# Kernel tuning notes

Hardware: AMD Instinct MI355X
Metric: run time of the kernel (lower is better)

The kernel has to match this reference:

```python
import jax, jax.numpy as jnp
import numpy as np

DIM = 2048
HEAD_DIM = 128
H = DIM // HEAD_DIM          # num ttt heads = 16
D_H = 128                    # inter_multi = 1.0 -> d_h = head_dim
CHUNK = 2048                 # lact_chunk_size
B, L = 1, 8192
BASE_LR = 0.01
LN_EPS = 1e-6                # flax LayerNorm default
NS_COEFS = [(4.0848, -6.8946, 2.927), (3.9505, -6.3029, 2.6377),
            (3.7418, -5.5913, 2.3037), (2.8769, -3.1427, 1.2046),
            (2.8366, -3.0525, 1.2012)]


def silu(x):
    return x * jax.nn.sigmoid(x)


def silu_backprop(dy, x):
    s = jax.nn.sigmoid(x)
    return dy * s * (1 + x * (1 - s))


def l2_norm(x, eps=1e-5):
    return x / (jnp.linalg.norm(x, axis=-1, keepdims=True) + eps)


def zeropower_ns5(G):
    # 5-step Newton-Schulz orthogonalization on a batch of matrices (bh, m, n)
    X = G
    transposed = G.shape[1] > G.shape[2]
    if transposed:
        X = jnp.swapaxes(X, 1, 2)
    X = X / (jnp.linalg.norm(X, axis=(1, 2), keepdims=True) + 1e-7)
    for a, b, c in NS_COEFS:
        A = X @ jnp.swapaxes(X, 1, 2)
        Bm = b * A + c * (A @ A)
        X = a * X + Bm @ X
    if transposed:
        X = jnp.swapaxes(X, 1, 2)
    return X


def block_causal_lact_swiglu(w0, w1, w2, q, k, v, lr0, lr1, lr2, momentum):
    # w0,w2: (bh, d_h, d); w1: (bh, d, d_h); q,k,v: (bh, l, d); lr*: (bh, l, 1)
    bh, l, d = k.shape
    v = jnp.swapaxes(v, 1, 2)   # (bh, d, l)
    q = jnp.swapaxes(q, 1, 2)   # (bh, d, l)
    w0_norm = jnp.linalg.norm(w0, axis=2, keepdims=True)
    w1_norm = jnp.linalg.norm(w1, axis=2, keepdims=True)
    w2_norm = jnp.linalg.norm(w2, axis=2, keepdims=True)
    outs = []
    for i in range(0, l - CHUNK, CHUNK):
        s, e = i, i + CHUNK
        ki = k[:, s:e, :]                      # (bh, C, d)
        vi = v[:, :, s:e]                      # (bh, d, C)
        qi = q[:, :, s:e]                      # (bh, d, C)
        lr0i, lr1i, lr2i = lr0[:, s:e, :], lr1[:, s:e, :], lr2[:, s:e, :]
        # apply current fast weights to queries
        h = w2 @ qi                            # (bh, d_h, C)
        gate = silu(w0 @ qi)
        outs.append(w1 @ (gate * h))           # (bh, d, C)
        # manual SwiGLU backprop through keys to get fast-weight grads
        kiT = jnp.swapaxes(ki, 1, 2)           # (bh, d, C)
        gate_before = w0 @ kiT                 # (bh, d_h, C)
        hidden_before = w2 @ kiT               # (bh, d_h, C)
        hidden = silu(gate_before) * hidden_before
        dhidden = jnp.swapaxes(w1, 1, 2) @ vi  # (bh, d_h, C)
        dhidden_before = dhidden * silu(gate_before)
        dgate = dhidden * hidden_before
        dgate_before = silu_backprop(dgate, gate_before)
        lr1iT = jnp.swapaxes(lr1i, 1, 2)       # (bh, 1, C) per-token lr
        dw1 = vi @ jnp.swapaxes(hidden * lr1iT, 1, 2)   # (bh, d, d_h)
        dw0 = dgate_before @ (ki * lr0i)                # (bh, d_h, d)
        dw2 = dhidden_before @ (ki * lr2i)              # (bh, d_h, d)
        if momentum is not None:
            m_i = jnp.mean(momentum[:, s:e, :], axis=1, keepdims=True)  # (bh,1,1)
            dw0 = dw0 + dw0 * m_i
            dw1 = dw1 + dw1 * m_i
            dw2 = dw2 + dw2 * m_i
        dw0 = zeropower_ns5(dw0)
        dw1 = zeropower_ns5(dw1)
        dw2 = zeropower_ns5(dw2)
        w0 = w0 + dw0
        w1 = w1 + dw1
        w2 = w2 + dw2
        # renormalize rows back to the initial norms
        w0 = w0 / (jnp.linalg.norm(w0, axis=2, keepdims=True) + 1e-5) * w0_norm
        w1 = w1 / (jnp.linalg.norm(w1, axis=2, keepdims=True) + 1e-5) * w1_norm
        w2 = w2 / (jnp.linalg.norm(w2, axis=2, keepdims=True) + 1e-5) * w2_norm
    # final chunk: apply only
    qi = q[:, :, l - CHUNK:]
    h = w2 @ qi
    gate = silu(w0 @ qi)
    outs.append(w1 @ (gate * h))
    out = jnp.concatenate(outs, axis=2)        # (bh, d, l)
    return jnp.swapaxes(out, 1, 2)             # (bh, l, d)


def _forward(x, W_qkv, W_lr, W_o, W_m, b_m, W_s, b_s, ln_g, ln_b, w0, w1, w2):
    b, l, _ = x.shape
    h, d = H, HEAD_DIM
    qkv = silu(x @ W_qkv).reshape(b, l, h, 3 * d)
    ttt_q, ttt_k, ttt_v = jnp.split(qkv, 3, axis=-1)
    ttt_q = l2_norm(ttt_q).reshape(b * h, l, d)
    ttt_k = l2_norm(ttt_k).reshape(b * h, l, d)
    ttt_v = ttt_v.reshape(b * h, l, d)
    base_lr_inv = BASE_LR + jnp.log(-jnp.expm1(jnp.float32(-BASE_LR)))
    lr = jax.nn.softplus(x @ W_lr + base_lr_inv)                 # (b, l, 3h)
    lr = lr.reshape(b, l, 3, h).transpose(2, 0, 3, 1).reshape(3, b * h, l, 1)
    lr0, lr1, lr2 = lr[0], lr[1], lr[2]
    w0b = jnp.tile(w0, (b, 1, 1))
    w1b = jnp.tile(w1, (b, 1, 1))
    w2b = jnp.tile(w2, (b, 1, 1))
    momentum = jax.nn.sigmoid(x @ W_m + b_m)                     # (b, l, h)
    momentum = momentum.reshape(b, l, h, 1).transpose(0, 2, 1, 3).reshape(b * h, l, 1)
    out = block_causal_lact_swiglu(w0b, w1b, w2b, ttt_q, ttt_k, ttt_v,
                                   lr0, lr1, lr2, momentum)      # (bh, l, d)
    # LayerNorm over last dim (flax default eps)
    mu = jnp.mean(out, axis=-1, keepdims=True)
    var = jnp.mean(jnp.square(out - mu), axis=-1, keepdims=True)
    out = (out - mu) * jax.lax.rsqrt(var + LN_EPS) * ln_g + ln_b
    scale = silu(x @ W_s + b_s).reshape(b, l, h, 1).transpose(0, 2, 1, 3).reshape(b * h, l, 1)
    out = out * scale
    out = out.reshape(b, h, l, d).transpose(0, 2, 1, 3).reshape(b, l, h * d)
    return out @ W_o


def setup_inputs() -> dict:
    ks = jax.random.split(jax.random.key(0), 11)
    sd = 1.0 / np.sqrt(DIM)
    return {
        "x": jax.random.normal(ks[0], (B, L, DIM), jnp.float32),
        "W_qkv": jax.random.normal(ks[1], (DIM, 3 * DIM), jnp.float32) * sd,
        "W_lr": jax.random.normal(ks[2], (DIM, 3 * H), jnp.float32) * sd,
        "W_o": jax.random.normal(ks[3], (DIM, DIM), jnp.float32) * sd,
        "W_m": jax.random.normal(ks[4], (DIM, H), jnp.float32) * sd,
        "b_m": jnp.zeros((H,), jnp.float32),
        "W_s": jax.random.normal(ks[5], (DIM, H), jnp.float32) * sd,
        "b_s": jnp.zeros((H,), jnp.float32),
        "ln_g": jnp.ones((HEAD_DIM,), jnp.float32),
        "ln_b": jnp.zeros((HEAD_DIM,), jnp.float32),
        "w0": jax.random.normal(ks[6], (H, D_H, HEAD_DIM), jnp.float32) / np.sqrt(HEAD_DIM),
        "w1": jax.random.normal(ks[7], (H, HEAD_DIM, D_H), jnp.float32) / np.sqrt(D_H),
        "w2": jax.random.normal(ks[8], (H, D_H, HEAD_DIM), jnp.float32) / np.sqrt(HEAD_DIM),
    }


def reference(x, W_qkv, W_lr, W_o, W_m, b_m, W_s, b_s, ln_g, ln_b, w0, w1, w2):
    return _forward(x, W_qkv, W_lr, W_o, W_m, b_m, W_s, b_s, ln_g, ln_b, w0, w1, w2)
```

## Files before the change

### kernel.cpp

```cpp
#include <hip/hip_runtime.h>
#include <hip/hip_bf16.h>
#include <cstdint>
#include <cstddef>

#define LSEQ   8192
#define DMODEL 2048
#define NH     16
#define HD     128
#define CH     2048

typedef __attribute__((ext_vector_type(8))) __bf16 bf16x8;
typedef __attribute__((ext_vector_type(4))) float f32x4;


__device__ __forceinline__ float wave_sum64(float v) {
#pragma unroll
  for (int m = 32; m; m >>= 1) v += __shfl_xor(v, m, 64);
  return v;
}

__device__ __forceinline__ float sigm(float x) { return 1.0f / (1.0f + expf(-x)); }

__device__ __forceinline__ unsigned short f2bf(float f) {
  unsigned int u = __float_as_uint(f);
  u += 0x7FFFu + ((u >> 16) & 1u);
  return (unsigned short)(u >> 16);
}
__device__ __forceinline__ float bf2f(unsigned short h) {
  return __uint_as_float((unsigned int)h << 16);
}

__device__ __forceinline__ void gload_lds16(const void* g, void* l) {
  __builtin_amdgcn_global_load_lds((__attribute__((address_space(1))) void*)(g),
                                   (__attribute__((address_space(3))) void*)(l), 16, 0, 0);
}


__global__ void k_cast(const float* __restrict__ X, unsigned short* __restrict__ Xb, int n4) {
  int i = blockIdx.x * 256 + threadIdx.x;
  int stride = gridDim.x * 256;
  for (; i < n4; i += stride) {
    float4 v = ((const float4*)X)[i];
    ushort4 o;
    o.x = f2bf(v.x); o.y = f2bf(v.y); o.z = f2bf(v.z); o.w = f2bf(v.w);
    ((ushort4*)Xb)[i] = o;
  }
}

__global__ void k_tcast(const float* __restrict__ W, unsigned short* __restrict__ Wt,
                        int K, int N) {
  __shared__ float t[64][65];
  const int n0 = blockIdx.x * 64, k0 = blockIdx.y * 64;
  const int tid = threadIdx.x;
  const int cx = tid & 63, ry = tid >> 6;
#pragma unroll
  for (int r = 0; r < 16; ++r) {
    int row = ry + r * 4;
    t[row][cx] = W[(size_t)(k0 + row) * N + n0 + cx];
  }
  __syncthreads();
#pragma unroll
  for (int r = 0; r < 16; ++r) {
    int nn = ry + r * 4;
    Wt[(size_t)(n0 + nn) * K + k0 + cx] = f2bf(t[cx][nn]);
  }
}


__device__ __forceinline__ void gemm_core(const unsigned short* __restrict__ A,
                                          const unsigned short* __restrict__ B,
                                          int K, int ldA, int ldB, int row0, int col0,
                                          unsigned short* Al, unsigned short* Bl,
                                          f32x4 acc[4][4]) {
  const int tid = threadIdx.x;
  const int w = tid >> 6, l = tid & 63;
  const int lrow = l & 15, lk = (l >> 4) * 8;
  const int wr = (w >> 1) * 64, wc = (w & 1) * 64;
  const int srow = l >> 2, skk = (l & 3) * 8;

  for (int kk = 0; kk < K; kk += 32) {
#pragma unroll
    for (int q = 0; q < 2; ++q) {
      int c = w * 2 + q;
      gload_lds16(A + (size_t)(row0 + c * 16 + srow) * ldA + kk + skk, &Al[c * 512]);
      gload_lds16(B + (size_t)(col0 + c * 16 + srow) * ldB + kk + skk, &Bl[c * 512]);
    }
    __syncthreads();
    bf16x8 af[4], bfr[4];
#pragma unroll
    for (int m = 0; m < 4; ++m)
      af[m] = *(const bf16x8*)&Al[(wr + m * 16 + lrow) * 32 + lk];
#pragma unroll
    for (int n = 0; n < 4; ++n)
      bfr[n] = *(const bf16x8*)&Bl[(wc + n * 16 + lrow) * 32 + lk];
#pragma unroll
    for (int m = 0; m < 4; ++m)
#pragma unroll
      for (int n = 0; n < 4; ++n)
        acc[m][n] = __builtin_amdgcn_mfma_f32_16x16x32_bf16(af[m], bfr[n], acc[m][n], 0, 0, 0);
    __syncthreads();
  }
}


__device__ __forceinline__ bf16x8 ld_sw(const unsigned short* base, int row, int kcol) {
  int byte = (row * 256 + kcol * 2) ^ ((row & 7) << 4);
  return *(const bf16x8*)((const char*)base + byte);
}
__device__ __forceinline__ void st_sw(unsigned short* base, int row, int col, unsigned short v) {
  int byte = (row * 256 + col * 2) ^ ((row & 7) << 4);
  *(unsigned short*)((char*)base + byte) = v;
}

__device__ __forceinline__ void stage_sw(const float* __restrict__ src, int ld,
                                         unsigned short* dst, int tid) {
#pragma unroll
  for (int p = 0; p < 16; ++p) {
    int row = p * 8 + (tid >> 5);
    int col = (tid & 31) * 4;
    float4 v = *(const float4*)(src + (size_t)row * ld + col);
    int byte = (row * 256 + col * 2) ^ ((row & 7) << 4);
    unsigned short* d = (unsigned short*)((char*)dst + byte);
    d[0] = f2bf(v.x); d[1] = f2bf(v.y); d[2] = f2bf(v.z); d[3] = f2bf(v.w);
  }
}

__device__ __forceinline__ void stage_hl(const float* __restrict__ src, int ld,
                                         unsigned short* H, unsigned short* L, int tid) {
#pragma unroll
  for (int p = 0; p < 16; ++p) {
    int row = p * 8 + (tid >> 5);
    int col = (tid & 31) * 4;
    float4 v = *(const float4*)(src + (size_t)row * ld + col);
    int byte = (row * 256 + col * 2) ^ ((row & 7) << 4);
    unsigned short* h = (unsigned short*)((char*)H + byte);
    unsigned short* l = (unsigned short*)((char*)L + byte);
    const float* pv = (const float*)&v;
#pragma unroll
    for (int i = 0; i < 4; ++i) {
      unsigned short hi = f2bf(pv[i]);
      h[i] = hi;
      l[i] = f2bf(pv[i] - bf2f(hi));
    }
  }
}

__device__ __forceinline__ void stage_hl_t(const float* __restrict__ src, int ld,
                                           unsigned short* H, unsigned short* L, int tid) {
#pragma unroll
  for (int p = 0; p < 16; ++p) {
    int k = p * 8 + (tid >> 5);
    int c = (tid & 31) * 4;
    float4 v = *(const float4*)(src + (size_t)k * ld + c);
    const float* pv = (const float*)&v;
#pragma unroll
    for (int i = 0; i < 4; ++i) {
      unsigned short hi = f2bf(pv[i]);
      st_sw(H, c + i, k, hi);
      st_sw(L, c + i, k, f2bf(pv[i] - bf2f(hi)));
    }
  }
}

__device__ __forceinline__ void stage_hl_ts(const float* __restrict__ src, int ld,
                                            const float* __restrict__ lr,
                                            unsigned short* H, unsigned short* L, int tid) {
#pragma unroll
  for (int p = 0; p < 16; ++p) {
    int t = p * 8 + (tid >> 5);
    int d = (tid & 31) * 4;
    float4 v = *(const float4*)(src + (size_t)t * ld + d);
    float sc = lr[t];
    const float* pv = (const float*)&v;
#pragma unroll
    for (int i = 0; i < 4; ++i) {
      float x = pv[i] * sc;
      unsigned short hi = f2bf(x);
      st_sw(H, d + i, t, hi);
      st_sw(L, d + i, t, f2bf(x - bf2f(hi)));
    }
  }
}


__global__ void k_init_w(const float* __restrict__ w0, const float* __restrict__ w1,
                         const float* __restrict__ w2, float* __restrict__ WW,
                         float* __restrict__ WN0) {
  int rid = blockIdx.x;
  int m = rid >> 11;
  int gr = rid & 2047;
  const float* src = (m == 0) ? w0 : (m == 1) ? w1 : w2;
  const float* row = src + (size_t)gr * HD;
  float* drow = WW + ((size_t)m * 2048 + gr) * HD;
  int l = threadIdx.x;
  float v0 = row[l], v1 = row[l + 64];
  drow[l] = v0; drow[l + 64] = v1;
  float s = wave_sum64(v0 * v0 + v1 * v1);
  if (l == 0) WN0[rid] = sqrtf(s);
}


__global__ __launch_bounds__(256) void k_qkv_mfma(const unsigned short* __restrict__ xb,
                                                  const unsigned short* __restrict__ Wqt,
                                                  float* __restrict__ Q, float* __restrict__ Km,
                                                  float* __restrict__ V) {
  __shared__ unsigned short Al[128 * 32];
  __shared__ unsigned short Bl[128 * 32];
  f32x4 acc[4][4];
#pragma unroll
  for (int m = 0; m < 4; ++m)
#pragma unroll
    for (int n = 0; n < 4; ++n) acc[m][n] = {};

  gemm_core(xb, Wqt, DMODEL, DMODEL, DMODEL, blockIdx.x * 128, blockIdx.y * 128, Al, Bl, acc);

  const int ct = blockIdx.y, hh = ct / 3, which = ct % 3;
  float* dst = (which == 0) ? Q : (which == 1) ? Km : V;
  const int tid = threadIdx.x, w = tid >> 6, l = tid & 63;
  const int wr = (w >> 1) * 64, wc = (w & 1) * 64;
#pragma unroll
  for (int m = 0; m < 4; ++m)
#pragma unroll
    for (int j = 0; j < 4; ++j) {
      int t = blockIdx.x * 128 + wr + m * 16 + (l >> 4) * 4 + j;
      int fth = t * NH + hh;
      int g = fth >> 13, tp = fth & 8191;
      float* drow = dst + ((size_t)g * LSEQ + tp) * HD;
#pragma unroll
      for (int n = 0; n < 4; ++n) {
        float v = acc[m][n][j];
        drow[wc + n * 16 + (l & 15)] = v * sigm(v);
      }
    }
}

__global__ void k_l2norm(float* __restrict__ Q, float* __restrict__ Km) {
  int rid = blockIdx.x * 4 + (threadIdx.x >> 6);
  int l = threadIdx.x & 63;
  float* base = (rid < NH * LSEQ) ? Q : Km;
  int r = (rid < NH * LSEQ) ? rid : rid - NH * LSEQ;
  float* row = base + (size_t)r * HD;
  float v0 = row[l], v1 = row[l + 64];
  float s = wave_sum64(v0 * v0 + v1 * v1);
  float f = 1.0f / (sqrtf(s) + 1e-5f);
  row[l] = v0 * f;
  row[l + 64] = v1 * f;
}


// ... 150 lines not shown
    for (int m = 0; m < 4; ++m)
#pragma unroll
      for (int n = 0; n < 4; ++n)
        oa[m][n] = __builtin_amdgcn_mfma_f32_16x16x32_bf16(af[m], b1[n], oa[m][n], 0, 0, 0);
  }
  __syncthreads();
#pragma unroll
  for (int m = 0; m < 4; ++m)
#pragma unroll
    for (int n = 0; n < 4; ++n)
#pragma unroll
      for (int j = 0; j < 4; ++j) {
        int row = wr + m * 16 + (l >> 4) * 4 + j;
        int col = wc + n * 16 + (l & 15);
        Os[row * 132 + col] = oa[m][n][j];
      }
  __syncthreads();

  const int tok = tid >> 1, part = tid & 1;
  const float* orow = Os + tok * 132 + part * 64;
  float sum = 0.0f;
#pragma unroll
  for (int q = 0; q < 16; ++q) {
    float4 v = *(const float4*)(orow + q * 4);
    sum += (v.x + v.y) + (v.z + v.w);
  }
  sum += __shfl_xor(sum, 1, 64);
  float mu = sum * (1.0f / 128.0f);
  float vs = 0.0f;
#pragma unroll
  for (int q = 0; q < 16; ++q) {
    float4 v = *(const float4*)(orow + q * 4);
    float d0 = v.x - mu, d1 = v.y - mu, d2 = v.z - mu, d3 = v.w - mu;
    vs += d0 * d0 + d1 * d1 + d2 * d2 + d3 * d3;
  }
  vs += __shfl_xor(vs, 1, 64);
  float rstd = rsqrtf(vs * (1.0f / 128.0f) + 1e-6f);
  int tabs = s + t0 + tok;
  float sc = SCL[(size_t)g * LSEQ + tabs];
  unsigned short* urow = U + (size_t)tabs * DMODEL + g * HD + part * 64;
#pragma unroll
  for (int q = 0; q < 16; ++q) {
    float4 v = *(const float4*)(orow + q * 4);
    int d = part * 64 + q * 4;
    ushort4 o;
    o.x = f2bf(((v.x - mu) * rstd * lng[d + 0] + lnb[d + 0]) * sc);
    o.y = f2bf(((v.y - mu) * rstd * lng[d + 1] + lnb[d + 1]) * sc);
    o.z = f2bf(((v.z - mu) * rstd * lng[d + 2] + lnb[d + 2]) * sc);
    o.w = f2bf(((v.w - mu) * rstd * lng[d + 3] + lnb[d + 3]) * sc);
    *(ushort4*)(urow + q * 4) = o;
  }
}


__global__ __launch_bounds__(256) void k_front_mx(const float* __restrict__ WW,
                                                  const float* __restrict__ Km,
                                                  const float* __restrict__ V,
                                                  float* __restrict__ BUF, int s) {
  __shared__ __align__(16) char smem[131072];
  unsigned short* AH = (unsigned short*)smem;
  unsigned short* AL = (unsigned short*)(smem + 32768);
  unsigned short* BH = (unsigned short*)(smem + 65536);
  unsigned short* BL = (unsigned short*)(smem + 98304);

  const int tt0 = blockIdx.x * 128;
  const int g = blockIdx.y;
  const int z = blockIdx.z;
  const int tid = threadIdx.x;
  const int w = tid >> 6, l = tid & 63;
  const int lrow = l & 15, lk8 = (l >> 4) * 8;
  const int wr = (w >> 1) * 64, wc = (w & 1) * 64;

  const int wsel = (z == 0) ? 0 : (z == 1) ? 2 : 1;
  const float* wg = WW + ((size_t)wsel * 2048 + g * 128) * 128;
  const float* X = (z == 2) ? V : Km;

  if (z != 2) stage_hl(wg, 128, AH, AL, tid);
  else        stage_hl_t(wg, 128, AH, AL, tid);
  stage_hl(X + ((size_t)g * LSEQ + s + tt0) * HD, HD, BH, BL, tid);
  __syncthreads();

  f32x4 acc[4][4];
#pragma unroll
  for (int m = 0; m < 4; ++m)
#pragma unroll
    for (int n = 0; n < 4; ++n) acc[m][n] = {};
#pragma unroll
  for (int kk = 0; kk < 128; kk += 32) {
    bf16x8 ah[4], al4[4], bh[4], bl4[4];
#pragma unroll
    for (int m = 0; m < 4; ++m) {
      ah[m] = ld_sw(AH, wr + m * 16 + lrow, kk + lk8);
      al4[m] = ld_sw(AL, wr + m * 16 + lrow, kk + lk8);
    }
#pragma unroll
    for (int n = 0; n < 4; ++n) {
      bh[n] = ld_sw(BH, wc + n * 16 + lrow, kk + lk8);
      bl4[n] = ld_sw(BL, wc + n * 16 + lrow, kk + lk8);
    }
#pragma unroll
    for (int m = 0; m < 4; ++m)
#pragma unroll
      for (int n = 0; n < 4; ++n) {
        acc[m][n] = __builtin_amdgcn_mfma_f32_16x16x32_bf16(ah[m], bh[n], acc[m][n], 0, 0, 0);
        acc[m][n] = __builtin_amdgcn_mfma_f32_16x16x32_bf16(ah[m], bl4[n], acc[m][n], 0, 0, 0);
        acc[m][n] = __builtin_amdgcn_mfma_f32_16x16x32_bf16(al4[m], bh[n], acc[m][n], 0, 0, 0);
      }
  }

  float* out = BUF + (size_t)z * (NH * 128 * CH) + (size_t)g * 128 * CH;
#pragma unroll
  for (int m = 0; m < 4; ++m)
#pragma unroll
    for (int n = 0; n < 4; ++n)
#pragma unroll
      for (int j = 0; j < 4; ++j) {
        int row = wr + m * 16 + (l >> 4) * 4 + j;
        int col = wc + n * 16 + (l & 15);
        out[(size_t)row * CH + tt0 + col] = acc[m][n][j];
      }
}

__global__ void k_elem(float* __restrict__ BA, float* __restrict__ BB, float* __restrict__ BC) {
  size_t i = ((size_t)blockIdx.x * 256 + threadIdx.x) * 4;
  float4 a = *(const float4*)(BA + i);
  float4 b = *(const float4*)(BB + i);
  float4 c = *(const float4*)(BC + i);
  float4 ha, hb2, hc;
  float* pa = (float*)&a; float* pb = (float*)&b; float* pc = (float*)&c;
  float* oa = (float*)&ha; float* ob = (float*)&hb2; float* oc = (float*)&hc;
#pragma unroll
  for (int k = 0; k < 4; ++k) {
    float gb = pa[k], hb = pb[k], dh = pc[k];
    float sg = sigm(gb);
    float sgb = gb * sg;
    float hid = sgb * hb;
    float dgate = dh * hb;
    float dgb = dgate * sg * (1.0f + gb * (1.0f - sg));
    float dhb = dh * sgb;
    oa[k] = hid; ob[k] = dgb; oc[k] = dhb;
  }
  *(float4*)(BA + i) = ha;
  *(float4*)(BB + i) = hb2;
  *(float4*)(BC + i) = hc;
}

__global__ __launch_bounds__(256) void k_dwp_mx(const float* __restrict__ BUF,
                                                const float* __restrict__ Km,
                                                const float* __restrict__ V,
                                                const float* __restrict__ LR,
                                                float* __restrict__ DWP, int s) {
  __shared__ __align__(16) char smem[131072];
  unsigned short* AH = (unsigned short*)smem;
  unsigned short* AL = (unsigned short*)(smem + 32768);
  unsigned short* BH = (unsigned short*)(smem + 65536);
  unsigned short* BL = (unsigned short*)(smem + 98304);

  const int p = blockIdx.x;
  const int g = blockIdx.y;
  const int z = blockIdx.z;
  const int tid = threadIdx.x;
  const int w = tid >> 6, l = tid & 63;
  const int lrow = l & 15, lk8 = (l >> 4) * 8;
  const int wr = (w >> 1) * 64, wc = (w & 1) * 64;

  const int msel = (z == 0) ? 1 : (z == 1) ? 0 : 2;
  const float* M = BUF + (size_t)msel * (NH * 128 * CH) + (size_t)g * 128 * CH;
  const float* N = (z == 1) ? V : Km;
  const float* lr = LR + (size_t)(z * NH + g) * LSEQ;
  const int ts = p * 256;

  f32x4 acc[4][4];
#pragma unroll
  for (int m = 0; m < 4; ++m)
#pragma unroll
    for (int n = 0; n < 4; ++n) acc[m][n] = {};

  for (int h = 0; h < 2; ++h) {
    if (h) __syncthreads();
    stage_hl(M + ts + h * 128, CH, AH, AL, tid);
    stage_hl_ts(N + ((size_t)g * LSEQ + s + ts + h * 128) * HD, HD,
                lr + s + ts + h * 128, BH, BL, tid);
    __syncthreads();
#pragma unroll
    for (int kk = 0; kk < 128; kk += 32) {
      bf16x8 ah[4], al4[4], bh[4], bl4[4];
#pragma unroll
      for (int m = 0; m < 4; ++m) {
        ah[m] = ld_sw(AH, wr + m * 16 + lrow, kk + lk8);
        al4[m] = ld_sw(AL, wr + m * 16 + lrow, kk + lk8);
      }
#pragma unroll
      for (int n = 0; n < 4; ++n) {
        bh[n] = ld_sw(BH, wc + n * 16 + lrow, kk + lk8);
        bl4[n] = ld_sw(BL, wc + n * 16 + lrow, kk + lk8);
      }
#pragma unroll
      for (int m = 0; m < 4; ++m)
#pragma unroll
        for (int n = 0; n < 4; ++n) {
          acc[m][n] = __builtin_amdgcn_mfma_f32_16x16x32_bf16(ah[m], bh[n], acc[m][n], 0, 0, 0);
          acc[m][n] = __builtin_amdgcn_mfma_f32_16x16x32_bf16(ah[m], bl4[n], acc[m][n], 0, 0, 0);
          acc[m][n] = __builtin_amdgcn_mfma_f32_16x16x32_bf16(al4[m], bh[n], acc[m][n], 0, 0, 0);
        }
    }
  }

  float* outp = DWP + (((size_t)(z * NH + g)) * 8 + p) * 16384;
#pragma unroll
  for (int m = 0; m < 4; ++m)
#pragma unroll
    for (int n = 0; n < 4; ++n)
#pragma unroll
      for (int j = 0; j < 4; ++j) {
        int row = wr + m * 16 + (l >> 4) * 4 + j;
        int col = wc + n * 16 + (l & 15);
        outp[row * 128 + col] = acc[m][n][j];
      }
}

__global__ void k_dwred(const float* __restrict__ DWP, float* __restrict__ DW) {
  int zg = blockIdx.x;
  int z = zg >> 4;
  const float* base = DWP + (size_t)zg * 8 * 16384;
  float* out = DW + (size_t)zg * 16384;
  for (int idx = threadIdx.x; idx < 16384; idx += 256) {
    float sv = 0.0f;
#pragma unroll
    for (int pp = 0; pp < 8; ++pp) sv += base[(size_t)pp * 16384 + idx];
    int oidx = (z == 1) ? ((idx & 127) * 128 + (idx >> 7)) : idx;
    out[oidx] = sv;
  }
}


__global__ __launch_bounds__(1024) void k_ns5(float* __restrict__ DW) {
  __shared__ float Xs[128 * 128];
  __shared__ float Aw[128 * 128];
  const float NA[5] = {4.0848f, 3.9505f, 3.7418f, 2.8769f, 2.8366f};
  const float NB[5] = {-6.8946f, -6.3029f, -5.5913f, -3.1427f, -3.0525f};
  const float NC[5] = {2.927f, 2.6377f, 2.3037f, 1.2046f, 1.2012f};
  float* Gm = DW + (size_t)blockIdx.x * 16384;
  const int tid = threadIdx.x;
  const int ty = tid >> 5, tx = tid & 31;

  float psum = 0.0f;
#pragma unroll
  for (int r = 0; r < 16; ++r) {
    int idx = tid + r * 1024;
    float v = Gm[idx];
    Xs[idx] = v;
    psum = fmaf(v, v, psum);
  }
  psum = wave_sum64(psum);
  if ((tid & 63) == 0) Aw[tid >> 6] = psum;
  __syncthreads();
  if (tid == 0) {
    float tot = 0.0f;
    for (int i = 0; i < 16; ++i) tot += Aw[i];
    Aw[0] = 1.0f / (sqrtf(tot) + 1e-7f);
  }
  __syncthreads();
  float scl = Aw[0];
#pragma unroll
  for (int r = 0; r < 16; ++r) {
    int idx = tid + r * 1024;
    Xs[idx] *= scl;
  }
  __syncthreads();

#pragma unroll 1
  for (int it = 0; it < 5; ++it) {
    float ac = NA[it], bc = NB[it], cc = NC[it];
#pragma unroll
    for (int ii = 0; ii < 4; ++ii)
#pragma unroll
      for (int jj = 0; jj < 4; ++jj)
        Aw[(tx * 4 + jj) * 128 + ty * 4 + ii] = Xs[(ty * 4 + ii) * 128 + tx * 4 + jj];
    __syncthreads();
    float Ar[4][4];
#pragma unroll
    for (int ii = 0; ii < 4; ++ii)
#pragma unroll
      for (int jj = 0; jj < 4; ++jj) Ar[ii][jj] = 0.0f;
    for (int k = 0; k < 128; ++k) {
      float a[4], b[4];
#pragma unroll
      for (int ii = 0; ii < 4; ++ii) a[ii] = Xs[(ty * 4 + ii) * 128 + k];
#pragma unroll
      for (int jj = 0; jj < 4; ++jj) b[jj] = Aw[k * 128 + tx * 4 + jj];
#pragma unroll
      for (int ii = 0; ii < 4; ++ii)
#pragma unroll
        for (int jj = 0; jj < 4; ++jj) Ar[ii][jj] = fmaf(a[ii], b[jj], Ar[ii][jj]);
    }
    __syncthreads();
#pragma unroll
    for (int ii = 0; ii < 4; ++ii)
#pragma unroll
      for (int jj = 0; jj < 4; ++jj)
        Aw[(ty * 4 + ii) * 128 + tx * 4 + jj] = Ar[ii][jj];
    __syncthreads();
    float Bm[4][4];
#pragma unroll
    for (int ii = 0; ii < 4; ++ii)
#pragma unroll
      for (int jj = 0; jj < 4; ++jj) Bm[ii][jj] = 0.0f;
    for (int k = 0; k < 128; ++k) {
      float a[4], b[4];
#pragma unroll
      for (int ii = 0; ii < 4; ++ii) a[ii] = Aw[(ty * 4 + ii) * 128 + k];
#pragma unroll
      for (int jj = 0; jj < 4; ++jj) b[jj] = Aw[k * 128 + tx * 4 + jj];
#pragma unroll
      for (int ii = 0; ii < 4; ++ii)
#pragma unroll
        for (int jj = 0; jj < 4; ++jj) Bm[ii][jj] = fmaf(a[ii], b[jj], Bm[ii][jj]);
    }
#pragma unroll
    for (int ii = 0; ii < 4; ++ii)
#pragma unroll
      for (int jj = 0; jj < 4; ++jj) Bm[ii][jj] = fmaf(bc, Ar[ii][jj], cc * Bm[ii][jj]);
    __syncthreads();
#pragma unroll
    for (int ii = 0; ii < 4; ++ii)
#pragma unroll
      for (int jj = 0; jj < 4; ++jj)
        Aw[(ty * 4 + ii) * 128 + tx * 4 + jj] = Bm[ii][jj];
    __syncthreads();
    float Xn[4][4];
#pragma unroll
    for (int ii = 0; ii < 4; ++ii)
#pragma unroll
      for (int jj = 0; jj < 4; ++jj)
        Xn[ii][jj] = ac * Xs[(ty * 4 + ii) * 128 + tx * 4 + jj];
    for (int k = 0; k < 128; ++k) {
      float a[4], b[4];
#pragma unroll
      for (int ii = 0; ii < 4; ++ii) a[ii] = Aw[(ty * 4 + ii) * 128 + k];
#pragma unroll
      for (int jj = 0; jj < 4; ++jj) b[jj] = Xs[k * 128 + tx * 4 + jj];
#pragma unroll
      for (int ii = 0; ii < 4; ++ii)
#pragma unroll
        for (int jj = 0; jj < 4; ++jj) Xn[ii][jj] = fmaf(a[ii], b[jj], Xn[ii][jj]);
    }
    __syncthreads();
#pragma unroll
    for (int ii = 0; ii < 4; ++ii)
#pragma unroll
      for (int jj = 0; jj < 4; ++jj)
        Xs[(ty * 4 + ii) * 128 + tx * 4 + jj] = Xn[ii][jj];
    __syncthreads();
  }
#pragma unroll
  for (int r = 0; r < 16; ++r) {
    int idx = tid + r * 1024;
    Gm[idx] = Xs[idx];
  }
}

__global__ void k_apply(float* __restrict__ WW, const float* __restrict__ DW,
                        const float* __restrict__ WN0) {
  int rid = blockIdx.x;
  int l = threadIdx.x;
  float* wrow = WW + (size_t)rid * 128;
  const float* drow = DW + (size_t)rid * 128;
  float v0 = wrow[l] + drow[l];
  float v1 = wrow[l + 64] + drow[l + 64];
  float s = wave_sum64(v0 * v0 + v1 * v1);
  float f = WN0[rid] / (sqrtf(s) + 1e-5f);
  wrow[l] = v0 * f;
  wrow[l + 64] = v1 * f;
}


__global__ __launch_bounds__(256) void k_final_mfma(const unsigned short* __restrict__ U,
                                                    const unsigned short* __restrict__ Wot,
                                                    float* __restrict__ out) {
  __shared__ unsigned short Al[128 * 32];
  __shared__ unsigned short Bl[128 * 32];
  f32x4 acc[4][4];
#pragma unroll
  for (int m = 0; m < 4; ++m)
#pragma unroll
    for (int n = 0; n < 4; ++n) acc[m][n] = {};

  const int row0 = blockIdx.x * 128, col0 = blockIdx.y * 128;
  gemm_core(U, Wot, DMODEL, DMODEL, DMODEL, row0, col0, Al, Bl, acc);

  const int tid = threadIdx.x, w = tid >> 6, l = tid & 63;
  const int wr = (w >> 1) * 64, wc = (w & 1) * 64;
#pragma unroll
  for (int m = 0; m < 4; ++m)
#pragma unroll
    for (int j = 0; j < 4; ++j) {
      int t = row0 + wr + m * 16 + (l >> 4) * 4 + j;
      float* orow = out + (size_t)t * DMODEL + col0;
#pragma unroll
      for (int n = 0; n < 4; ++n)
        orow[wc + n * 16 + (l & 15)] = acc[m][n][j];
    }
}


extern "C" void kernel_launch(void* const* d_in, const int* in_sizes, int n_in,
                              void* d_out, int out_size, void* d_ws, size_t ws_size,
                              hipStream_t stream) {
  (void)in_sizes; (void)n_in; (void)out_size;
  const float* x    = (const float*)d_in[0];
  const float* Wqkv = (const float*)d_in[1];
  const float* Wlr  = (const float*)d_in[2];
  const float* Wo   = (const float*)d_in[3];
  const float* Wsc  = (const float*)d_in[6];
  const float* bs   = (const float*)d_in[7];
  const float* lng  = (const float*)d_in[8];
  const float* lnb  = (const float*)d_in[9];
  const float* w0   = (const float*)d_in[10];
  const float* w1   = (const float*)d_in[11];
  const float* w2   = (const float*)d_in[12];

  float* Q = (float*)d_out;

  float* ws = (float*)d_ws;
  size_t off = 0;
  auto alloc = [&](size_t n) { float* p = ws + off; off += n; return p; };
  float* Km   = alloc((size_t)NH * LSEQ * HD);
  float* V    = alloc((size_t)NH * LSEQ * HD);
  float* Uf   = alloc((size_t)LSEQ * DMODEL / 2);
  float* LR   = alloc((size_t)3 * NH * LSEQ);
  float* SCL  = alloc((size_t)NH * LSEQ);
  float* WW   = alloc((size_t)3 * NH * HD * HD);
  float* WN0  = alloc((size_t)3 * NH * HD);
  float* BUF  = alloc((size_t)3 * NH * HD * CH);
  float* DW   = alloc((size_t)3 * NH * HD * HD);
  float* DWP  = alloc((size_t)3 * NH * 8 * HD * HD);
  if (off * sizeof(float) > ws_size) return;

  unsigned short* U = (unsigned short*)Uf;
  unsigned short* xb  = (unsigned short*)BUF;
  unsigned short* Wqt = (unsigned short*)(BUF + (size_t)LSEQ * DMODEL / 2);
  float* Plr = BUF;
  unsigned short* Wot = (unsigned short*)BUF;

  k_init_w<<<3 * NH * HD, 64, 0, stream>>>(w0, w1, w2, WW, WN0);
  k_cast<<<2048, 256, 0, stream>>>(x, xb, LSEQ * DMODEL / 4);
  k_tcast<<<dim3(3 * DMODEL / 64, DMODEL / 64), 256, 0, stream>>>(Wqkv, Wqt, DMODEL, 3 * DMODEL);
  k_qkv_mfma<<<dim3(LSEQ / 128, 48), 256, 0, stream>>>(xb, Wqt, Q, Km, V);
  k_l2norm<<<2 * NH * LSEQ / 4, 256, 0, stream>>>(Q, Km);
  k_lrms5<<<dim3(LSEQ / 64, 16), 256, 0, stream>>>(x, Wlr, Wsc, Plr);
  k_lrsum<<<LSEQ * 64 / 256, 256, 0, stream>>>(Plr, bs, LR, SCL);

  for (int c = 0; c < 4; ++c) {
    int s = c * CH;
    k_out2<<<dim3(CH / 128, NH), 256, 0, stream>>>(WW, Q, SCL, lng, lnb, U, s);
    if (c < 3) {
      k_front_mx<<<dim3(CH / 128, NH, 3), 256, 0, stream>>>(WW, Km, V, BUF, s);
      k_elem<<<(NH * HD * CH) / (256 * 4), 256, 0, stream>>>(
          BUF, BUF + (size_t)NH * HD * CH, BUF + (size_t)2 * NH * HD * CH);
      k_dwp_mx<<<dim3(8, NH, 3), 256, 0, stream>>>(BUF, Km, V, LR, DWP, s);
      k_dwred<<<3 * NH, 256, 0, stream>>>(DWP, DW);
      k_ns5<<<3 * NH, 1024, 0, stream>>>(DW);
      k_apply<<<3 * NH * HD, 64, 0, stream>>>(WW, DW, WN0);
    }
  }
  k_tcast<<<dim3(DMODEL / 64, DMODEL / 64), 256, 0, stream>>>(Wo, Wot, DMODEL, DMODEL);
  k_final_mfma<<<dim3(LSEQ / 128, DMODEL / 128), 256, 0, stream>>>(U, Wot, (float*)d_out);
}
```

Baseline: 1.594 ms.

## Fuse front GEMMs with SwiGLU elementwise and move NS5 onto MFMA

Merges the three front-pass GEMMs (w0·k, w2·k, w1ᵀ·v) into one 1024-thread kernel. That kernel computes the SwiGLU forward and backward elementwise terms in registers, which removes the separate k_elem pass and its global round trip over BUF. A transposed copy of w1 is kept up to date in init and apply so the w1 operand can be read row-major. The Newton-Schulz orthogonalization is rewritten from scalar FP32 LDS matmuls to bf16 hi/lo split MFMA, which trades some precision for matrix-core throughput. The NS5 kernel also adds an in-LDS transpose each iteration.

```diff
diff --git a/kernel.cpp b/kernel.cpp
--- a/kernel.cpp
+++ b/kernel.cpp
@@ -34,6 +34,8 @@
   __builtin_amdgcn_global_load_lds((__attribute__((address_space(1))) void*)(g),
                                    (__attribute__((address_space(3))) void*)(l), 16, 0, 0);
 }
+
+union bfu8 { bf16x8 v; unsigned short u[8]; };
 
 
 __global__ void k_cast(const float* __restrict__ X, unsigned short* __restrict__ Xb, int n4) {
@@ -111,6 +113,10 @@
   int byte = (row * 256 + col * 2) ^ ((row & 7) << 4);
   *(unsigned short*)((char*)base + byte) = v;
 }
+__device__ __forceinline__ unsigned short ld_sw1(const unsigned short* base, int row, int col) {
+  int byte = (row * 256 + col * 2) ^ ((row & 7) << 4);
+  return *(const unsigned short*)((const char*)base + byte);
+}
 
 __device__ __forceinline__ void stage_sw(const float* __restrict__ src, int ld,
                                          unsigned short* dst, int tid) {
@@ -145,19 +151,22 @@
   }
 }
 
-__device__ __forceinline__ void stage_hl_t(const float* __restrict__ src, int ld,
-                                           unsigned short* H, unsigned short* L, int tid) {
-#pragma unroll
-  for (int p = 0; p < 16; ++p) {
-    int k = p * 8 + (tid >> 5);
-    int c = (tid & 31) * 4;
-    float4 v = *(const float4*)(src + (size_t)k * ld + c);
+__device__ __forceinline__ void stage_hl_1024(const float* __restrict__ src, int ld,
+                                              unsigned short* H, unsigned short* L, int tid) {
+#pragma unroll
+  for (int p = 0; p < 4; ++p) {
+    int row = p * 32 + (tid >> 5);
+    int col = (tid & 31) * 4;
+    float4 v = *(const float4*)(src + (size_t)row * ld + col);
+    int byte = (row * 256 + col * 2) ^ ((row & 7) << 4);
+    unsigned short* h = (unsigned short*)((char*)H + byte);
+    unsigned short* l = (unsigned short*)((char*)L + byte);
     const float* pv = (const float*)&v;
 #pragma unroll
     for (int i = 0; i < 4; ++i) {
       unsigned short hi = f2bf(pv[i]);
-      st_sw(H, c + i, k, hi);
-      st_sw(L, c + i, k, f2bf(pv[i] - bf2f(hi)));
+      h[i] = hi;
+      l[i] = f2bf(pv[i] - bf2f(hi));
     }
   }
 }
@@ -185,7 +194,7 @@
 
 __global__ void k_init_w(const float* __restrict__ w0, const float* __restrict__ w1,
                          const float* __restrict__ w2, float* __restrict__ WW,
-                         float* __restrict__ WN0) {
+                         float* __restrict__ WN0, float* __restrict__ W1T) {
   int rid = blockIdx.x;
   int m = rid >> 11;
   int gr = rid & 2047;
@@ -195,6 +204,11 @@
   int l = threadIdx.x;
   float v0 = row[l], v1 = row[l + 64];
   drow[l] = v0; drow[l + 64] = v1;
+  if (m == 1) {
+    int g = gr >> 7, r = gr & 127;
+    W1T[((size_t)g * 128 + l) * 128 + r] = v0;
+    W1T[((size_t)g * 128 + l + 64) * 128 + r] = v1;
+  }
   float s = wave_sum64(v0 * v0 + v1 * v1);
   if (l == 0) WN0[rid] = sqrtf(s);
 }
@@ -451,97 +465,107 @@
   }
 }
 
-
-__global__ __launch_bounds__(256) void k_front_mx(const float* __restrict__ WW,
-                                                  const float* __restrict__ Km,
-                                                  const float* __restrict__ V,
-                                                  float* __restrict__ BUF, int s) {
+__global__ __launch_bounds__(1024) void k_fe(const float* __restrict__ WW,
+                                             const float* __restrict__ W1T,
+                                             const float* __restrict__ Km,
+                                             const float* __restrict__ V,
+                                             float* __restrict__ BUF, int s) {
   __shared__ __align__(16) char smem[131072];
-  unsigned short* AH = (unsigned short*)smem;
-  unsigned short* AL = (unsigned short*)(smem + 32768);
-  unsigned short* BH = (unsigned short*)(smem + 65536);
-  unsigned short* BL = (unsigned short*)(smem + 98304);
+  unsigned short* KH = (unsigned short*)smem;
+  unsigned short* KL = (unsigned short*)(smem + 32768);
+  unsigned short* VH = (unsigned short*)(smem + 65536);
+  unsigned short* VL = (unsigned short*)(smem + 98304);
 
   const int tt0 = blockIdx.x * 128;
   const int g = blockIdx.y;
-  const int z = blockIdx.z;
   const int tid = threadIdx.x;
   const int w = tid >> 6, l = tid & 63;
+  const int ww = w >> 2, wv = w & 3;
   const int lrow = l & 15, lk8 = (l >> 4) * 8;
-  const int wr = (w >> 1) * 64, wc = (w & 1) * 64;
-
-  const int wsel = (z == 0) ? 0 : (z == 1) ? 2 : 1;
-  const float* wg = WW + ((size_t)wsel * 2048 + g * 128) * 128;
-  const float* X = (z == 2) ? V : Km;
-
-  if (z != 2) stage_hl(wg, 128, AH, AL, tid);
-  else        stage_hl_t(wg, 128, AH, AL, tid);
-  stage_hl(X + ((size_t)g * LSEQ + s + tt0) * HD, HD, BH, BL, tid);
-  __syncthreads();
-
-  f32x4 acc[4][4];
-#pragma unroll
-  for (int m = 0; m < 4; ++m)
-#pragma unroll
-    for (int n = 0; n < 4; ++n) acc[m][n] = {};
-#pragma unroll
-  for (int kk = 0; kk < 128; kk += 32) {
-    bf16x8 ah[4], al4[4], bh[4], bl4[4];
-#pragma unroll
-    for (int m = 0; m < 4; ++m) {
-      ah[m] = ld_sw(AH, wr + m * 16 + lrow, kk + lk8);
-      al4[m] = ld_sw(AL, wr + m * 16 + lrow, kk + lk8);
-    }
-#pragma unroll
-    for (int n = 0; n < 4; ++n) {
-      bh[n] = ld_sw(BH, wc + n * 16 + lrow, kk + lk8);
-      bl4[n] = ld_sw(BL, wc + n * 16 + lrow, kk + lk8);
-    }
-#pragma unroll
-    for (int m = 0; m < 4; ++m)
-#pragma unroll
-      for (int n = 0; n < 4; ++n) {
-        acc[m][n] = __builtin_amdgcn_mfma_f32_16x16x32_bf16(ah[m], bh[n], acc[m][n], 0, 0, 0);
-        acc[m][n] = __builtin_amdgcn_mfma_f32_16x16x32_bf16(ah[m], bl4[n], acc[m][n], 0, 0, 0);
-        acc[m][n] = __builtin_amdgcn_mfma_f32_16x16x32_bf16(al4[m], bh[n], acc[m][n], 0, 0, 0);
-      }
-  }
-
-  float* out = BUF + (size_t)z * (NH * 128 * CH) + (size_t)g * 128 * CH;
-#pragma unroll
-  for (int m = 0; m < 4; ++m)
-#pragma unroll
-    for (int n = 0; n < 4; ++n)
+  const int frow = (l >> 4) * 4, fcol = l & 15;
+
+  stage_hl_1024(Km + ((size_t)g * LSEQ + s + tt0) * HD, HD, KH, KL, tid);
+  stage_hl_1024(V + ((size_t)g * LSEQ + s + tt0) * HD, HD, VH, VL, tid);
+  __syncthreads();
+
+  const float* Asrc[3];
+  Asrc[0] = WW + ((size_t)0 * 2048 + g * 128) * 128;
+  Asrc[1] = WW + ((size_t)2 * 2048 + g * 128) * 128;
+  Asrc[2] = W1T + (size_t)g * 16384;
+
+  f32x4 acc[3][2][2];
+#pragma unroll
+  for (int q = 0; q < 3; ++q)
+#pragma unroll
+    for (int m = 0; m < 2; ++m)
+#pragma unroll
+      for (int n = 0; n < 2; ++n) acc[q][m][n] = {};
+
+#pragma unroll 1
+  for (int q = 0; q < 3; ++q) {
+    const float* src = Asrc[q];
+    const unsigned short* BH = (q == 2) ? VH : KH;
+    const unsigned short* BL = (q == 2) ? VL : KL;
+#pragma unroll
+    for (int kk = 0; kk < 128; kk += 32) {
+      bf16x8 ah[2], al[2], bh[2], bl[2];
+#pragma unroll
+      for (int m = 0; m < 2; ++m) {
+        int row = ww * 32 + m * 16 + lrow;
+        float4 v0 = *(const float4*)(src + (size_t)row * 128 + kk + lk8);
+        float4 v1 = *(const float4*)(src + (size_t)row * 128 + kk + lk8 + 4);
+        bfu8 h, lo;
+        const float* p0 = (const float*)&v0;
+        const float* p1 = (const float*)&v1;
+#pragma unroll
+        for (int i = 0; i < 4; ++i) {
+          unsigned short hb0 = f2bf(p0[i]);
+          h.u[i] = hb0; lo.u[i] = f2bf(p0[i] - bf2f(hb0));
+          unsigned short hb1 = f2bf(p1[i]);
+          h.u[i + 4] = hb1; lo.u[i + 4] = f2bf(p1[i] - bf2f(hb1));
+        }
+        ah[m] = h.v; al[m] = lo.v;
+      }
+#pragma unroll
+      for (int n = 0; n < 2; ++n) {
+        int row = wv * 32 + n * 16 + lrow;
+        bh[n] = ld_sw(BH, row, kk + lk8);
+        bl[n] = ld_sw(BL, row, kk + lk8);
+      }
+#pragma unroll
+      for (int m = 0; m < 2; ++m)
+#pragma unroll
+        for (int n = 0; n < 2; ++n) {
+          acc[q][m][n] = __builtin_amdgcn_mfma_f32_16x16x32_bf16(ah[m], bh[n], acc[q][m][n], 0, 0, 0);
+          acc[q][m][n] = __builtin_amdgcn_mfma_f32_16x16x32_bf16(ah[m], bl[n], acc[q][m][n], 0, 0, 0);
+          acc[q][m][n] = __builtin_amdgcn_mfma_f32_16x16x32_bf16(al[m], bh[n], acc[q][m][n], 0, 0, 0);
+        }
+    }
+  }
+
+  float* out0 = BUF + (size_t)0 * (NH * 128 * CH) + (size_t)g * 128 * CH;
+  float* out1 = BUF + (size_t)1 * (NH * 128 * CH) + (size_t)g * 128 * CH;
+  float* out2 = BUF + (size_t)2 * (NH * 128 * CH) + (size_t)g * 128 * CH;
+#pragma unroll
+  for (int m = 0; m < 2; ++m)
+#pragma unroll
+    for (int n = 0; n < 2; ++n)
 #pragma unroll
       for (int j = 0; j < 4; ++j) {
-        int row = wr + m * 16 + (l >> 4) * 4 + j;
-        int col = wc + n * 16 + (l & 15);
-        out[(size_t)row * CH + tt0 + col] = acc[m][n][j];
-      }
-}
-
-__global__ void k_elem(float* __restrict__ BA, float* __restrict__ BB, float* __restrict__ BC) {
-  size_t i = ((size_t)blockIdx.x * 256 + threadIdx.x) * 4;
-  float4 a = *(const float4*)(BA + i);
-  float4 b = *(const float4*)(BB + i);
-  float4 c = *(const float4*)(BC + i);
-  float4 ha, hb2, hc;
-  float* pa = (float*)&a; float* pb = (float*)&b; float* pc = (float*)&c;
-  float* oa = (float*)&ha; float* ob = (float*)&hb2; float* oc = (float*)&hc;
-#pragma unroll
-  for (int k = 0; k < 4; ++k) {
-    float gb = pa[k], hb = pb[k], dh = pc[k];
-    float sg = sigm(gb);
-    float sgb = gb * sg;
-    float hid = sgb * hb;
-    float dgate = dh * hb;
-    float dgb = dgate * sg * (1.0f + gb * (1.0f - sg));
-    float dhb = dh * sgb;
-    oa[k] = hid; ob[k] = dgb; oc[k] = dhb;
-  }
-  *(float4*)(BA + i) = ha;
-  *(float4*)(BB + i) = hb2;
-  *(float4*)(BC + i) = hc;
+        int row = ww * 32 + m * 16 + frow + j;
+        int col = wv * 32 + n * 16 + fcol;
+        float gb = acc[0][m][n][j];
+        float hb = acc[1][m][n][j];
+        float dh = acc[2][m][n][j];
+        float sg = sigm(gb);
+        float sgb = gb * sg;
+        float hid = sgb * hb;
+        float dgate = dh * hb;
+        float dgb = dgate * sg * (1.0f + gb * (1.0f - sg));
+        float dhb = dh * sgb;
+        size_t o = (size_t)row * CH + tt0 + col;
+        out0[o] = hid; out1[o] = dgb; out2[o] = dhb;
+      }
 }
 
 __global__ __launch_bounds__(256) void k_dwp_mx(const float* __restrict__ BUF,
@@ -632,136 +656,230 @@
   }
 }
 
-
-__global__ __launch_bounds__(1024) void k_ns5(float* __restrict__ DW) {
-  __shared__ float Xs[128 * 128];
-  __shared__ float Aw[128 * 128];
+__global__ __launch_bounds__(1024) void k_ns5_mfma(float* __restrict__ DW) {
+  __shared__ __align__(16) char smem[131072];
+  unsigned short* PH = (unsigned short*)smem;
+  unsigned short* PL = (unsigned short*)(smem + 32768);
+  unsigned short* QH = (unsigned short*)(smem + 65536);
+  unsigned short* QL = (unsigned short*)(smem + 98304);
+  float* red = (float*)(smem + 65536);
+
   const float NA[5] = {4.0848f, 3.9505f, 3.7418f, 2.8769f, 2.8366f};
   const float NB[5] = {-6.8946f, -6.3029f, -5.5913f, -3.1427f, -3.0525f};
   const float NC[5] = {2.927f, 2.6377f, 2.3037f, 1.2046f, 1.2012f};
   float* Gm = DW + (size_t)blockIdx.x * 16384;
   const int tid = threadIdx.x;
-  const int ty = tid >> 5, tx = tid & 31;
-
+  const int w = tid >> 6, l = tid & 63;
+  const int ww = w >> 2, wv = w & 3;
+  const int lrow = l & 15, lk8 = (l >> 4) * 8;
+  const int frow = (l >> 4) * 4, fcol = l & 15;
+
+  float vals[16];
   float psum = 0.0f;
+#pragma unroll
+  for (int r = 0; r < 16; ++r) {
+    vals[r] = Gm[tid + r * 1024];
+    psum = fmaf(vals[r], vals[r], psum);
+  }
+  psum = wave_sum64(psum);
+  if (l == 0) red[w] = psum;
+  __syncthreads();
+  float tot = 0.0f;
+#pragma unroll
+  for (int i = 0; i < 16; ++i) tot += red[i];
+  float scl = 1.0f / (sqrtf(tot) + 1e-7f);
+  __syncthreads();
 #pragma unroll
   for (int r = 0; r < 16; ++r) {
     int idx = tid + r * 1024;
-    float v = Gm[idx];
-    Xs[idx] = v;
-    psum = fmaf(v, v, psum);
-  }
-  psum = wave_sum64(psum);
-  if ((tid & 63) == 0) Aw[tid >> 6] = psum;
-  __syncthreads();
-  if (tid == 0) {
-    float tot = 0.0f;
-    for (int i = 0; i < 16; ++i) tot += Aw[i];
-    Aw[0] = 1.0f / (sqrtf(tot) + 1e-7f);
-  }
-  __syncthreads();
-  float scl = Aw[0];
+    int rr = idx >> 7, cc = idx & 127;
+    float v = vals[r] * scl;
+    unsigned short hi = f2bf(v);
+    st_sw(PH, rr, cc, hi);
+    st_sw(PL, rr, cc, f2bf(v - bf2f(hi)));
+  }
+  __syncthreads();
+
+#pragma unroll 1
+  for (int it = 0; it < 5; ++it) {
+    const float ac = NA[it], bc = NB[it], cc2 = NC[it];
+
+    f32x4 accA[2][2];
+#pragma unroll
+    for (int m = 0; m < 2; ++m)
+#pragma unroll
+      for (int n = 0; n < 2; ++n) accA[m][n] = {};
+#pragma unroll
+    for (int kk = 0; kk < 128; kk += 32) {
+      bf16x8 ah[2], al[2], bh[2], bl[2];
+#pragma unroll
+      for (int m = 0; m < 2; ++m) {
+        ah[m] = ld_sw(PH, ww * 32 + m * 16 + lrow, kk + lk8);
+        al[m] = ld_sw(PL, ww * 32 + m * 16 + lrow, kk + lk8);
+      }
+#pragma unroll
+      for (int n = 0; n < 2; ++n) {
+        bh[n] = ld_sw(PH, wv * 32 + n * 16 + lrow, kk + lk8);
+        bl[n] = ld_sw(PL, wv * 32 + n * 16 + lrow, kk + lk8);
+      }
+#pragma unroll
+      for (int m = 0; m < 2; ++m)
+#pragma unroll
+        for (int n = 0; n < 2; ++n) {
+          accA[m][n] = __builtin_amdgcn_mfma_f32_16x16x32_bf16(ah[m], bh[n], accA[m][n], 0, 0, 0);
+          accA[m][n] = __builtin_amdgcn_mfma_f32_16x16x32_bf16(ah[m], bl[n], accA[m][n], 0, 0, 0);
+          accA[m][n] = __builtin_amdgcn_mfma_f32_16x16x32_bf16(al[m], bh[n], accA[m][n], 0, 0, 0);
+        }
+    }
+#pragma unroll
+    for (int m = 0; m < 2; ++m)
+#pragma unroll
+      for (int n = 0; n < 2; ++n)
+#pragma unroll
+        for (int j = 0; j < 4; ++j) {
+          int row = ww * 32 + m * 16 + frow + j;
+          int col = wv * 32 + n * 16 + fcol;
+          float v = accA[m][n][j];
+          unsigned short hi = f2bf(v);
+          st_sw(QH, row, col, hi);
+          st_sw(QL, row, col, f2bf(v - bf2f(hi)));
+        }
+    __syncthreads();
+
+    f32x4 accB[2][2];
+#pragma unroll
+    for (int m = 0; m < 2; ++m)
+#pragma unroll
+      for (int n = 0; n < 2; ++n) accB[m][n] = {};
+#pragma unroll
+    for (int kk = 0; kk < 128; kk += 32) {
+      bf16x8 ah[2], al[2], bh[2], bl[2];
+#pragma unroll
+      for (int m = 0; m < 2; ++m) {
+        ah[m] = ld_sw(QH, ww * 32 + m * 16 + lrow, kk + lk8);
+        al[m] = ld_sw(QL, ww * 32 + m * 16 + lrow, kk + lk8);
+      }
+#pragma unroll
+      for (int n = 0; n < 2; ++n) {
+        bh[n] = ld_sw(QH, wv * 32 + n * 16 + lrow, kk + lk8);
+        bl[n] = ld_sw(QL, wv * 32 + n * 16 + lrow, kk + lk8);
+      }
+#pragma unroll
+      for (int m = 0; m < 2; ++m)
+#pragma unroll
+        for (int n = 0; n < 2; ++n) {
+          accB[m][n] = __builtin_amdgcn_mfma_f32_16x16x32_bf16(ah[m], bh[n], accB[m][n], 0, 0, 0);
+          accB[m][n] = __builtin_amdgcn_mfma_f32_16x16x32_bf16(ah[m], bl[n], accB[m][n], 0, 0, 0);
+          accB[m][n] = __builtin_amdgcn_mfma_f32_16x16x32_bf16(al[m], bh[n], accB[m][n], 0, 0, 0);
+        }
+    }
+#pragma unroll
+    for (int m = 0; m < 2; ++m)
+#pragma unroll
+      for (int n = 0; n < 2; ++n)
+#pragma unroll
+        for (int j = 0; j < 4; ++j)
+          accB[m][n][j] = fmaf(bc, accA[m][n][j], cc2 * accB[m][n][j]);
+    __syncthreads();
+#pragma unroll
+    for (int m = 0; m < 2; ++m)
+#pragma unroll
+      for (int n = 0; n < 2; ++n)
+#pragma unroll
+        for (int j = 0; j < 4; ++j) {
+          int row = ww * 32 + m * 16 + frow + j;
+          int col = wv * 32 + n * 16 + fcol;
+          float v = accB[m][n][j];
+          unsigned short hi = f2bf(v);
+          st_sw(QH, row, col, hi);
+          st_sw(QL, row, col, f2bf(v - bf2f(hi)));
+        }
+    unsigned short th[16], tl[16];
+#pragma unroll
+    for (int r = 0; r < 16; ++r) {
+      int idx = tid + r * 1024;
+      int rr = idx >> 7, ccx = idx & 127;
+      th[r] = ld_sw1(PH, rr, ccx);
+      tl[r] = ld_sw1(PL, rr, ccx);
+    }
+    __syncthreads();
+#pragma unroll
+    for (int r = 0; r < 16; ++r) {
+      int idx = tid + r * 1024;
+      int rr = idx >> 7, ccx = idx & 127;
+      st_sw(PH, ccx, rr, th[r]);
+      st_sw(PL, ccx, rr, tl[r]);
+    }
+    __syncthreads();
+
+    f32x4 accC[2][2];
+#pragma unroll
+    for (int m = 0; m < 2; ++m)
+#pragma unroll
+      for (int n = 0; n < 2; ++n) accC[m][n] = {};
+#pragma unroll
+    for (int kk = 0; kk < 128; kk += 32) {
+      bf16x8 ah[2], al[2], bh[2], bl[2];
+#pragma unroll
+      for (int m = 0; m < 2; ++m) {
+        ah[m] = ld_sw(PH, ww * 32 + m * 16 + lrow, kk + lk8);
+        al[m] = ld_sw(PL, ww * 32 + m * 16 + lrow, kk + lk8);
+      }
+#pragma unroll
+      for (int n = 0; n < 2; ++n) {
+        bh[n] = ld_sw(QH, wv * 32 + n * 16 + lrow, kk + lk8);
+        bl[n] = ld_sw(QL, wv * 32 + n * 16 + lrow, kk + lk8);
+      }
+#pragma unroll
+      for (int m = 0; m < 2; ++m)
+#pragma unroll
+        for (int n = 0; n < 2; ++n) {
+          accC[m][n] = __builtin_amdgcn_mfma_f32_16x16x32_bf16(ah[m], bh[n], accC[m][n], 0, 0, 0);
+          accC[m][n] = __builtin_amdgcn_mfma_f32_16x16x32_bf16(ah[m], bl[n], accC[m][n], 0, 0, 0);
+          accC[m][n] = __builtin_amdgcn_mfma_f32_16x16x32_bf16(al[m], bh[n], accC[m][n], 0, 0, 0);
+        }
+    }
+#pragma unroll
+    for (int m = 0; m < 2; ++m)
+#pragma unroll
+      for (int n = 0; n < 2; ++n)
+#pragma unroll
+        for (int j = 0; j < 4; ++j) {
+          int row = ww * 32 + m * 16 + frow + j;
+          int col = wv * 32 + n * 16 + fcol;
+          float yv = bf2f(ld_sw1(PH, row, col)) + bf2f(ld_sw1(PL, row, col));
+          accC[m][n][j] = fmaf(ac, yv, accC[m][n][j]);
+        }
+    __syncthreads();
+#pragma unroll
+    for (int m = 0; m < 2; ++m)
+#pragma unroll
+      for (int n = 0; n < 2; ++n)
+#pragma unroll
+        for (int j = 0; j < 4; ++j) {
+          int row = ww * 32 + m * 16 + frow + j;
+          int col = wv * 32 + n * 16 + fcol;
+          float v = accC[m][n][j];
+          unsigned short hi = f2bf(v);
+          st_sw(PH, row, col, hi);
+          st_sw(PL, row, col, f2bf(v - bf2f(hi)));
+        }
+    __syncthreads();
+  }
+
 #pragma unroll
   for (int r = 0; r < 16; ++r) {
     int idx = tid + r * 1024;
-    Xs[idx] *= scl;
-  }
-  __syncthreads();
-
-#pragma unroll 1
-  for (int it = 0; it < 5; ++it) {
-    float ac = NA[it], bc = NB[it], cc = NC[it];
-#pragma unroll
-    for (int ii = 0; ii < 4; ++ii)
-#pragma unroll
-      for (int jj = 0; jj < 4; ++jj)
-        Aw[(tx * 4 + jj) * 128 + ty * 4 + ii] = Xs[(ty * 4 + ii) * 128 + tx * 4 + jj];
-    __syncthreads();
-    float Ar[4][4];
-#pragma unroll
-    for (int ii = 0; ii < 4; ++ii)
-#pragma unroll
-      for (int jj = 0; jj < 4; ++jj) Ar[ii][jj] = 0.0f;
-    for (int k = 0; k < 128; ++k) {
-      float a[4], b[4];
-#pragma unroll
-      for (int ii = 0; ii < 4; ++ii) a[ii] = Xs[(ty * 4 + ii) * 128 + k];
-#pragma unroll
-      for (int jj = 0; jj < 4; ++jj) b[jj] = Aw[k * 128 + tx * 4 + jj];
-#pragma unroll
-      for (int ii = 0; ii < 4; ++ii)
-#pragma unroll
-        for (int jj = 0; jj < 4; ++jj) Ar[ii][jj] = fmaf(a[ii], b[jj], Ar[ii][jj]);
-    }
-    __syncthreads();
-#pragma unroll
-    for (int ii = 0; ii < 4; ++ii)
-#pragma unroll
-      for (int jj = 0; jj < 4; ++jj)
-        Aw[(ty * 4 + ii) * 128 + tx * 4 + jj] = Ar[ii][jj];
-    __syncthreads();
-    float Bm[4][4];
-#pragma unroll
-    for (int ii = 0; ii < 4; ++ii)
-#pragma unroll
-      for (int jj = 0; jj < 4; ++jj) Bm[ii][jj] = 0.0f;
-    for (int k = 0; k < 128; ++k) {
-      float a[4], b[4];
-#pragma unroll
-      for (int ii = 0; ii < 4; ++ii) a[ii] = Aw[(ty * 4 + ii) * 128 + k];
-#pragma unroll
-      for (int jj = 0; jj < 4; ++jj) b[jj] = Aw[k * 128 + tx * 4 + jj];
-#pragma unroll
-      for (int ii = 0; ii < 4; ++ii)
-#pragma unroll
-        for (int jj = 0; jj < 4; ++jj) Bm[ii][jj] = fmaf(a[ii], b[jj], Bm[ii][jj]);
-    }
-#pragma unroll
-    for (int ii = 0; ii < 4; ++ii)
-#pragma unroll
-      for (int jj = 0; jj < 4; ++jj) Bm[ii][jj] = fmaf(bc, Ar[ii][jj], cc * Bm[ii][jj]);
-    __syncthreads();
-#pragma unroll
-    for (int ii = 0; ii < 4; ++ii)
-#pragma unroll
-      for (int jj = 0; jj < 4; ++jj)
-        Aw[(ty * 4 + ii) * 128 + tx * 4 + jj] = Bm[ii][jj];
-    __syncthreads();
-    float Xn[4][4];
-#pragma unroll
-    for (int ii = 0; ii < 4; ++ii)
-#pragma unroll
-      for (int jj = 0; jj < 4; ++jj)
-        Xn[ii][jj] = ac * Xs[(ty * 4 + ii) * 128 + tx * 4 + jj];
-    for (int k = 0; k < 128; ++k) {
-      float a[4], b[4];
-#pragma unroll
-      for (int ii = 0; ii < 4; ++ii) a[ii] = Aw[(ty * 4 + ii) * 128 + k];
-#pragma unroll
-      for (int jj = 0; jj < 4; ++jj) b[jj] = Xs[k * 128 + tx * 4 + jj];
-#pragma unroll
-      for (int ii = 0; ii < 4; ++ii)
-#pragma unroll
-        for (int jj = 0; jj < 4; ++jj) Xn[ii][jj] = fmaf(a[ii], b[jj], Xn[ii][jj]);
-    }
-    __syncthreads();
-#pragma unroll
-    for (int ii = 0; ii < 4; ++ii)
-#pragma unroll
-      for (int jj = 0; jj < 4; ++jj)
-        Xs[(ty * 4 + ii) * 128 + tx * 4 + jj] = Xn[ii][jj];
-    __syncthreads();
-  }
-#pragma unroll
-  for (int r = 0; r < 16; ++r) {
-    int idx = tid + r * 1024;
-    Gm[idx] = Xs[idx];
+    int rr = idx >> 7, ccx = idx & 127;
+    Gm[idx] = bf2f(ld_sw1(PH, ccx, rr)) + bf2f(ld_sw1(PL, ccx, rr));
   }
 }
 
 __global__ void k_apply(float* __restrict__ WW, const float* __restrict__ DW,
-                        const float* __restrict__ WN0) {
+                        const float* __restrict__ WN0, float* __restrict__ W1T) {
   int rid = blockIdx.x;
+  int m = rid >> 11;
+  int gr = rid & 2047;
   int l = threadIdx.x;
   float* wrow = WW + (size_t)rid * 128;
   const float* drow = DW + (size_t)rid * 128;
@@ -769,8 +887,14 @@
   float v1 = wrow[l + 64] + drow[l + 64];
   float s = wave_sum64(v0 * v0 + v1 * v1);
   float f = WN0[rid] / (sqrtf(s) + 1e-5f);
-  wrow[l] = v0 * f;
-  wrow[l + 64] = v1 * f;
+  v0 *= f; v1 *= f;
+  wrow[l] = v0;
+  wrow[l + 64] = v1;
+  if (m == 1) {
+    int g = gr >> 7, r = gr & 127;
+    W1T[((size_t)g * 128 + l) * 128 + r] = v0;
+    W1T[((size_t)g * 128 + l + 64) * 128 + r] = v1;
+  }
 }
 
 
@@ -831,6 +955,7 @@
   float* SCL  = alloc((size_t)NH * LSEQ);
   float* WW   = alloc((size_t)3 * NH * HD * HD);
   float* WN0  = alloc((size_t)3 * NH * HD);
+  float* W1T  = alloc((size_t)NH * HD * HD);
   float* BUF  = alloc((size_t)3 * NH * HD * CH);
   float* DW   = alloc((size_t)3 * NH * HD * HD);
   float* DWP  = alloc((size_t)3 * NH * 8 * HD * HD);
@@ -842,7 +967,7 @@
   float* Plr = BUF;
   unsigned short* Wot = (unsigned short*)BUF;
 
-  k_init_w<<<3 * NH * HD, 64, 0, stream>>>(w0, w1, w2, WW, WN0);
+  k_init_w<<<3 * NH * HD, 64, 0, stream>>>(w0, w1, w2, WW, WN0, W1T);
   k_cast<<<2048, 256, 0, stream>>>(x, xb, LSEQ * DMODEL / 4);
   k_tcast<<<dim3(3 * DMODEL / 64, DMODEL / 64), 256, 0, stream>>>(Wqkv, Wqt, DMODEL, 3 * DMODEL);
   k_qkv_mfma<<<dim3(LSEQ / 128, 48), 256, 0, stream>>>(xb, Wqt, Q, Km, V);
@@ -854,13 +979,11 @@
     int s = c * CH;
     k_out2<<<dim3(CH / 128, NH), 256, 0, stream>>>(WW, Q, SCL, lng, lnb, U, s);
     if (c < 3) {
-      k_front_mx<<<dim3(CH / 128, NH, 3), 256, 0, stream>>>(WW, Km, V, BUF, s);
-      k_elem<<<(NH * HD * CH) / (256 * 4), 256, 0, stream>>>(
-          BUF, BUF + (size_t)NH * HD * CH, BUF + (size_t)2 * NH * HD * CH);
+      k_fe<<<dim3(CH / 128, NH), 1024, 0, stream>>>(WW, W1T, Km, V, BUF, s);
       k_dwp_mx<<<dim3(8, NH, 3), 256, 0, stream>>>(BUF, Km, V, LR, DWP, s);
       k_dwred<<<3 * NH, 256, 0, stream>>>(DWP, DW);
-      k_ns5<<<3 * NH, 1024, 0, stream>>>(DW);
-      k_apply<<<3 * NH * HD, 64, 0, stream>>>(WW, DW, WN0);
+      k_ns5_mfma<<<3 * NH, 1024, 0, stream>>>(DW);
+      k_apply<<<3 * NH * HD, 64, 0, stream>>>(WW, DW, WN0, W1T);
     }
   }
   k_tcast<<<dim3(DMODEL / 64, DMODEL / 64), 256, 0, stream>>>(Wo, Wot, DMODEL, DMODEL);
```

Result: faster. 1.402 ms (-12.1%).
